# Performance work log

Hardware: AMD Instinct MI355X
Metric: run time of the kernel (lower is better)

The kernel has to match this reference:

```python
import jax, jax.numpy as jnp
import numpy as np

N = 600_000            # active input voxels
CIN, COUT = 64, 128    # IN_CHANNELS, NUM_BEV_FEATURES
B, Z, Y, X = 4, 16, 468, 468  # sparse grid (Waymo-like); conv halves Z
BN_EPS = 1e-5


def setup_inputs() -> dict:
    rng = np.random.default_rng(0)
    # unique active voxel coordinates
    lin = rng.choice(B * Z * Y * X, size=N, replace=False)
    b = lin // (Z * Y * X)
    r = lin % (Z * Y * X)
    z = r // (Y * X)
    r = r % (Y * X)
    y = r // X
    x = r % X
    # spconv rulebook for kernel (2,1,1), stride (2,1,1), pad 0:
    # tap id along z and output segment id from unique (b, z//2, y, x)
    kz = (z % 2).astype(np.int32)
    keys = ((b * (Z // 2) + z // 2) * Y + y) * X + x
    _, inv = np.unique(keys, return_inverse=True)
    out_ids = inv.astype(np.int32)
    n_out = np.int32(out_ids.max() + 1)

    key = jax.random.key(0)
    ks = jax.random.split(key, 6)
    return {
        "features": jax.random.normal(ks[0], (N, CIN), dtype=jnp.float32),
        "W": jax.random.normal(ks[1], (2, CIN, COUT), dtype=jnp.float32) * 0.05,
        "gamma": jax.random.uniform(ks[2], (COUT,), dtype=jnp.float32, minval=0.5, maxval=1.5),
        "beta": jax.random.normal(ks[3], (COUT,), dtype=jnp.float32) * 0.1,
        "running_mean": jax.random.normal(ks[4], (COUT,), dtype=jnp.float32) * 0.1,
        "running_var": jax.random.uniform(ks[5], (COUT,), dtype=jnp.float32, minval=0.5, maxval=1.5),
        "kz": jnp.asarray(kz),
        "out_ids": jnp.asarray(out_ids),
        "n_out": jnp.asarray(n_out),
    }


def reference(features, W, gamma, beta, running_mean, running_var, kz, out_ids, n_out):
    # gather-GEMM: one GEMM per kernel tap, select by tap id
    y0 = features @ W[0]                       # [N, COUT]
    y1 = features @ W[1]
    contrib = jnp.where((kz == 0)[:, None], y0, y1)
    # scatter-add into output voxels (padded to N segments for static shape)
    out = jax.ops.segment_sum(contrib, out_ids, num_segments=N)  # [N, COUT]
    # BatchNorm1d (eval) + ReLU, fused into scatter output pass
    inv_std = gamma * jax.lax.rsqrt(running_var + BN_EPS)
    out = jax.nn.relu((out - running_mean) * inv_std + beta)
    # zero out padding rows beyond the true number of output voxels
    valid = (jnp.arange(N) < n_out)[:, None]
    return jnp.where(valid, out, 0.0)
```

## Files before the change

kernel.cpp:

```cpp
#include <hip/hip_runtime.h>
#include <stdint.h>

#define CIN 64
#define COUT 128
#define TILE_ROWS 64
#define BLOCK 256
#define WT_STRIDE 136
#define A_STRIDE 136

typedef __attribute__((ext_vector_type(8))) __bf16 bf16x8;
typedef __attribute__((ext_vector_type(8))) unsigned short ushort8;
typedef __attribute__((ext_vector_type(4))) float f32x4;

__device__ __forceinline__ unsigned short f2bf(float f) {
    uint32_t u = __float_as_uint(f);
    u = (u + 0x7FFFu + ((u >> 16) & 1u)) >> 16;
    return (unsigned short)u;
}

__global__ void scatter_inv_kernel(const int* __restrict__ kz,
                                   const int* __restrict__ oid,
                                   int* __restrict__ inv0,
                                   int* __restrict__ inv1,
                                   int n) {
    int i = blockIdx.x * blockDim.x + threadIdx.x;
    if (i < n) {
        int o = oid[i];
        if (kz[i] == 0) inv0[o] = i + 1;
        else            inv1[o] = i + 1;
    }
}

__launch_bounds__(BLOCK)
__global__ void spconv_bn_relu_kernel(const float* __restrict__ feat,
                                      const float* __restrict__ W,
                                      const float* __restrict__ gamma,
                                      const float* __restrict__ beta,
                                      const float* __restrict__ rmean,
                                      const float* __restrict__ rvar,
                                      const int* __restrict__ inv0,
                                      const int* __restrict__ inv1,
                                      const int* __restrict__ n_out_p,
                                      float* __restrict__ out,
                                      int N, int num_tiles) {
    __shared__ unsigned short lds_wT[COUT * WT_STRIDE];
    __shared__ unsigned short lds_a[TILE_ROWS * A_STRIDE];
    __shared__ float lds_scale[COUT];
    __shared__ float lds_bias[COUT];

    const int tid = threadIdx.x;
    const int nout = *n_out_p;

    const float4* W4 = (const float4*)W;
    #pragma unroll
    for (int u = 0; u < 16; ++u) {
        int flat4 = u * BLOCK + tid;
        int n4 = flat4 & 31;
        int k  = flat4 >> 5;
        float4 v = W4[flat4];
        int nb = n4 * 4;
        lds_wT[(nb + 0) * WT_STRIDE + k] = f2bf(v.x);
        lds_wT[(nb + 1) * WT_STRIDE + k] = f2bf(v.y);
        lds_wT[(nb + 2) * WT_STRIDE + k] = f2bf(v.z);
        lds_wT[(nb + 3) * WT_STRIDE + k] = f2bf(v.w);
    }
    if (tid < COUT) {
        float s = gamma[tid] * rsqrtf(rvar[tid] + 1e-5f);
        lds_scale[tid] = s;
        lds_bias[tid]  = fmaf(-rmean[tid], s, beta[tid]);
    }
    __syncthreads();

    const float4* feat4 = (const float4*)feat;
    const int wave = tid >> 6;
    const int lane = tid & 63;
    const int lrow = lane & 15;
    const int quad = lane >> 4;

    for (int tile = blockIdx.x; tile < num_tiles; tile += gridDim.x) {
        const int tile_base = tile * TILE_ROWS;

        #pragma unroll
        for (int u = 0; u < 8; ++u) {
            int flat  = u * BLOCK + tid;
            int r     = flat >> 5;
            int rem   = flat & 31;
            int tap   = rem >> 4;
            int chunk = rem & 15;
            int o = tile_base + r;
            int idx = 0;
            if (o < N) idx = tap ? inv1[o] : inv0[o];
            float4 v = make_float4(0.f, 0.f, 0.f, 0.f);
            if (idx > 0) v = feat4[(size_t)(idx - 1) * 16 + chunk];
            uint2 p;
            p.x = (uint32_t)f2bf(v.x) | ((uint32_t)f2bf(v.y) << 16);
            p.y = (uint32_t)f2bf(v.z) | ((uint32_t)f2bf(v.w) << 16);
            *(uint2*)&lds_a[r * A_STRIDE + tap * 64 + chunk * 4] = p;
        }
        __syncthreads();

        const unsigned short* abase = &lds_a[(wave * 16 + lrow) * A_STRIDE + quad * 8];
        bf16x8 afrag[4];
        #pragma unroll
        for (int s = 0; s < 4; ++s)
            afrag[s] = __builtin_bit_cast(bf16x8, *(const ushort8*)(abase + s * 32));

        #pragma unroll
        for (int c = 0; c < 8; ++c) {
            const unsigned short* bbase = &lds_wT[(c * 16 + lrow) * WT_STRIDE + quad * 8];
            f32x4 acc = {0.f, 0.f, 0.f, 0.f};
            #pragma unroll
            for (int s = 0; s < 4; ++s) {
                bf16x8 bfrag = __builtin_bit_cast(bf16x8, *(const ushort8*)(bbase + s * 32));
                acc = __builtin_amdgcn_mfma_f32_16x16x32_bf16(afrag[s], bfrag, acc, 0, 0, 0);
            }
            int col = c * 16 + lrow;
            float sc = lds_scale[col];
            float bi = lds_bias[col];
            int rbase = tile_base + wave * 16 + quad * 4;
            #pragma unroll
            for (int reg = 0; reg < 4; ++reg) {
                int o = rbase + reg;
                if (o < N) {
                    float v = 0.f;
                    if (o < nout) v = fmaxf(fmaf(acc[reg], sc, bi), 0.f);
                    out[(size_t)o * COUT + col] = v;
                }
            }
        }
        __syncthreads();
    }
}

extern "C" void kernel_launch(void* const* d_in, const int* in_sizes, int n_in,
                              void* d_out, int out_size, void* d_ws, size_t ws_size,
                              hipStream_t stream) {
    const float* feat  = (const float*)d_in[0];
    const float* W     = (const float*)d_in[1];
    const float* gamma = (const float*)d_in[2];
    const float* beta  = (const float*)d_in[3];
    const float* rmean = (const float*)d_in[4];
    const float* rvar  = (const float*)d_in[5];
    const int*   kz    = (const int*)d_in[6];
    const int*   oid   = (const int*)d_in[7];
    const int*   noutp = (const int*)d_in[8];
    float* out = (float*)d_out;

    const int N = in_sizes[6];

    int* inv0 = (int*)d_ws;
    int* inv1 = inv0 + N;

    hipMemsetAsync(d_ws, 0, (size_t)2 * N * sizeof(int), stream);

    int sb = (N + 255) / 256;
    scatter_inv_kernel<<<sb, 256, 0, stream>>>(kz, oid, inv0, inv1, N);

    int num_tiles = (N + TILE_ROWS - 1) / TILE_ROWS;
    int grid = num_tiles < 1875 ? num_tiles : 1875;
    spconv_bn_relu_kernel<<<grid, BLOCK, 0, stream>>>(
        feat, W, gamma, beta, rmean, rvar, inv0, inv1, noutp, out, N, num_tiles);
}
```

Measured before the change: 560.8 us.

## Gather features directly into MFMA registers per wave, drop LDS staging and block syncs

Each wave now owns a 16-row tile and loads gathered feature rows straight from global memory into registers, converting them to bf16 fragments without an LDS staging buffer or __syncthreads. The MFMA operands are swapped so each lane holds four consecutive output columns and writes them as one float4 store. The next tile's inverse indices are prefetched while the current one computes. Grid size and launch bounds also change. The per-lane gathers are less coalesced (32-byte pieces per lane), which may cost memory efficiency in exchange for removing the LDS round-trip and the barriers.

```diff
diff --git a/kernel.cpp b/kernel.cpp
--- a/kernel.cpp
+++ b/kernel.cpp
@@ -3,10 +3,8 @@
 
 #define CIN 64
 #define COUT 128
-#define TILE_ROWS 64
 #define BLOCK 256
 #define WT_STRIDE 136
-#define A_STRIDE 136
 
 typedef __attribute__((ext_vector_type(8))) __bf16 bf16x8;
 typedef __attribute__((ext_vector_type(8))) unsigned short ushort8;
@@ -31,7 +29,7 @@
     }
 }
 
-__launch_bounds__(BLOCK)
+__launch_bounds__(BLOCK, 4)
 __global__ void spconv_bn_relu_kernel(const float* __restrict__ feat,
                                       const float* __restrict__ W,
                                       const float* __restrict__ gamma,
@@ -42,11 +40,10 @@
                                       const int* __restrict__ inv1,
                                       const int* __restrict__ n_out_p,
                                       float* __restrict__ out,
-                                      int N, int num_tiles) {
+                                      int N, int num_wtiles) {
     __shared__ unsigned short lds_wT[COUT * WT_STRIDE];
-    __shared__ unsigned short lds_a[TILE_ROWS * A_STRIDE];
-    __shared__ float lds_scale[COUT];
-    __shared__ float lds_bias[COUT];
+    __shared__ __align__(16) float lds_scale[COUT];
+    __shared__ __align__(16) float lds_bias[COUT];
 
     const int tid = threadIdx.x;
     const int nout = *n_out_p;
@@ -77,33 +74,48 @@
     const int lrow = lane & 15;
     const int quad = lane >> 4;
 
-    for (int tile = blockIdx.x; tile < num_tiles; tile += gridDim.x) {
-        const int tile_base = tile * TILE_ROWS;
+    const int gwave   = blockIdx.x * (BLOCK / 64) + wave;
+    const int wstride = gridDim.x * (BLOCK / 64);
 
+    int i0 = 0, i1 = 0;
+    if (gwave < num_wtiles) {
+        int row = gwave * 16 + lrow;
+        if (row < N) { i0 = inv0[row]; i1 = inv1[row]; }
+    }
+
+    for (int wt = gwave; wt < num_wtiles; wt += wstride) {
+        const int row = wt * 16 + lrow;
+
+        float4 ra[4], rb[4];
         #pragma unroll
-        for (int u = 0; u < 8; ++u) {
-            int flat  = u * BLOCK + tid;
-            int r     = flat >> 5;
-            int rem   = flat & 31;
-            int tap   = rem >> 4;
-            int chunk = rem & 15;
-            int o = tile_base + r;
-            int idx = 0;
-            if (o < N) idx = tap ? inv1[o] : inv0[o];
-            float4 v = make_float4(0.f, 0.f, 0.f, 0.f);
-            if (idx > 0) v = feat4[(size_t)(idx - 1) * 16 + chunk];
-            uint2 p;
-            p.x = (uint32_t)f2bf(v.x) | ((uint32_t)f2bf(v.y) << 16);
-            p.y = (uint32_t)f2bf(v.z) | ((uint32_t)f2bf(v.w) << 16);
-            *(uint2*)&lds_a[r * A_STRIDE + tap * 64 + chunk * 4] = p;
+        for (int s = 0; s < 4; ++s) {
+            int idx = (s < 2) ? i0 : i1;
+            ra[s] = make_float4(0.f, 0.f, 0.f, 0.f);
+            rb[s] = make_float4(0.f, 0.f, 0.f, 0.f);
+            if (idx > 0) {
+                const float4* p = feat4 + (size_t)(idx - 1) * 16 + (s & 1) * 8 + quad * 2;
+                ra[s] = p[0];
+                rb[s] = p[1];
+            }
         }
-        __syncthreads();
 
-        const unsigned short* abase = &lds_a[(wave * 16 + lrow) * A_STRIDE + quad * 8];
+        int nwt = wt + wstride;
+        int p0 = 0, p1 = 0;
+        if (nwt < num_wtiles) {
+            int nr = nwt * 16 + lrow;
+            if (nr < N) { p0 = inv0[nr]; p1 = inv1[nr]; }
+        }
+
         bf16x8 afrag[4];
         #pragma unroll
-        for (int s = 0; s < 4; ++s)
-            afrag[s] = __builtin_bit_cast(bf16x8, *(const ushort8*)(abase + s * 32));
+        for (int s = 0; s < 4; ++s) {
+            ushort8 u;
+            u[0] = f2bf(ra[s].x); u[1] = f2bf(ra[s].y);
+            u[2] = f2bf(ra[s].z); u[3] = f2bf(ra[s].w);
+            u[4] = f2bf(rb[s].x); u[5] = f2bf(rb[s].y);
+            u[6] = f2bf(rb[s].z); u[7] = f2bf(rb[s].w);
+            afrag[s] = __builtin_bit_cast(bf16x8, u);
+        }
 
         #pragma unroll
         for (int c = 0; c < 8; ++c) {
@@ -111,24 +123,25 @@
             f32x4 acc = {0.f, 0.f, 0.f, 0.f};
             #pragma unroll
             for (int s = 0; s < 4; ++s) {
-                bf16x8 bfrag = __builtin_bit_cast(bf16x8, *(const ushort8*)(bbase + s * 32));
-                acc = __builtin_amdgcn_mfma_f32_16x16x32_bf16(afrag[s], bfrag, acc, 0, 0, 0);
+                bf16x8 wfrag = __builtin_bit_cast(bf16x8, *(const ushort8*)(bbase + s * 32));
+                acc = __builtin_amdgcn_mfma_f32_16x16x32_bf16(wfrag, afrag[s], acc, 0, 0, 0);
             }
-            int col = c * 16 + lrow;
-            float sc = lds_scale[col];
-            float bi = lds_bias[col];
-            int rbase = tile_base + wave * 16 + quad * 4;
-            #pragma unroll
-            for (int reg = 0; reg < 4; ++reg) {
-                int o = rbase + reg;
-                if (o < N) {
-                    float v = 0.f;
-                    if (o < nout) v = fmaxf(fmaf(acc[reg], sc, bi), 0.f);
-                    out[(size_t)o * COUT + col] = v;
+            if (row < N) {
+                const int col = c * 16 + quad * 4;
+                float4 o4 = make_float4(0.f, 0.f, 0.f, 0.f);
+                if (row < nout) {
+                    f32x4 sc = *(const f32x4*)&lds_scale[col];
+                    f32x4 bi = *(const f32x4*)&lds_bias[col];
+                    o4.x = fmaxf(fmaf(acc[0], sc[0], bi[0]), 0.f);
+                    o4.y = fmaxf(fmaf(acc[1], sc[1], bi[1]), 0.f);
+                    o4.z = fmaxf(fmaf(acc[2], sc[2], bi[2]), 0.f);
+                    o4.w = fmaxf(fmaf(acc[3], sc[3], bi[3]), 0.f);
                 }
+                *(float4*)&out[(size_t)row * COUT + col] = o4;
             }
         }
-        __syncthreads();
+
+        i0 = p0; i1 = p1;
     }
 }
 
@@ -156,8 +169,9 @@
     int sb = (N + 255) / 256;
     scatter_inv_kernel<<<sb, 256, 0, stream>>>(kz, oid, inv0, inv1, N);
 
-    int num_tiles = (N + TILE_ROWS - 1) / TILE_ROWS;
-    int grid = num_tiles < 1875 ? num_tiles : 1875;
+    int num_wtiles = (N + 15) / 16;
+    int nblocks = (num_wtiles + 3) / 4;
+    int grid = nblocks < 1024 ? nblocks : 1024;
     spconv_bn_relu_kernel<<<grid, BLOCK, 0, stream>>>(
-        feat, W, gamma, beta, rmean, rvar, inv0, inv1, noutp, out, N, num_tiles);
+        feat, W, gamma, beta, rmean, rvar, inv0, inv1, noutp, out, N, num_wtiles);
 }
```

Measured after the change: 567.3 us. Within noise of the previous version (+1.2%).
